# Performance work log

Measured on AMD Instinct MI355X. Metric: run time of the kernel, lower is better.

The kernel has to match this reference:

```python
import jax, jax.numpy as jnp
import numpy as np

NUM_HEADS = 8
NUM_GROUPS = 8
NUM_ITERATIONS = 3
DT = 0.1
EPS = 1e-5


def group_norm(x, scale, bias):
    # x: [B, C, H, W], GroupNorm(8, C)
    B, C, H, W = x.shape
    xg = x.reshape(B, NUM_GROUPS, C // NUM_GROUPS, H, W)
    mean = xg.mean(axis=(2, 3, 4), keepdims=True)
    var = xg.var(axis=(2, 3, 4), keepdims=True)
    xg = (xg - mean) * jax.lax.rsqrt(var + EPS)
    x = xg.reshape(B, C, H, W)
    return x * scale[None, :, None, None] + bias[None, :, None, None]


def setup_inputs() -> dict:
    key = jax.random.key(0)
    ks = jax.random.split(key, 4)
    B, C, H, W = 8, 512, 32, 32
    x = jax.random.normal(ks[0], (B, C, H, W), dtype=jnp.float32)
    qkv_w = jax.random.normal(ks[1], (3 * C, C), dtype=jnp.float32) * (1.0 / np.sqrt(C))
    proj_w = jax.random.normal(ks[2], (C, C), dtype=jnp.float32) * (1.0 / np.sqrt(C))
    inl_w = jax.random.normal(ks[3], (C, C), dtype=jnp.float32) * (1.0 / np.sqrt(C))
    return {
        "x": x,
        "gn_scale": jnp.ones((C,), jnp.float32),
        "gn_bias": jnp.zeros((C,), jnp.float32),
        "qkv_w": qkv_w,
        "qkv_b": jnp.zeros((3 * C,), jnp.float32),
        "proj_w": proj_w,
        "proj_b": jnp.zeros((C,), jnp.float32),
        "inl_w": inl_w,
        "inl_b": jnp.zeros((C,), jnp.float32),
    }


def reference(x, gn_scale, gn_bias, qkv_w, qkv_b, proj_w, proj_b, inl_w, inl_b):
    B, C, H, W = x.shape
    nh = NUM_HEADS
    hd = C // nh
    S = H * W

    h = group_norm(x, gn_scale, gn_bias)

    # 1x1 conv == channel matmul
    qkv = jnp.einsum('oc,bchw->bohw', qkv_w, h) + qkv_b[None, :, None, None]
    q, k, v = jnp.split(qkv, 3, axis=1)  # each [B, C, H, W]

    def to_heads(t):  # [B, C, H, W] -> [B, nh, S, hd]
        return t.reshape(B, nh, hd, S).transpose(0, 1, 3, 2)

    q, k, v = to_heads(q), to_heads(k), to_heads(v)

    scale = hd ** (-0.5)
    attn = jax.nn.softmax(jnp.einsum('bnsd,bntd->bnst', q, k) * scale, axis=-1)
    h = jnp.einsum('bnst,bntd->bnsd', attn, v)  # [B, nh, S, hd]

    # back to [B, S, C] for INL refinement
    h_flat = h.transpose(0, 1, 3, 2).reshape(B, C, S).transpose(0, 2, 1)

    # SimpleINLDynamics: iterative Euler refinement x <- x + dt * tanh(W x + b)
    def step(hf, _):
        hf = hf + DT * jnp.tanh(jnp.einsum('bsc,oc->bso', hf, inl_w) + inl_b)
        return hf, None
    h_flat, _ = jax.lax.scan(step, h_flat, None, length=NUM_ITERATIONS)

    h = h_flat.transpose(0, 2, 1).reshape(B, C, H, W)
    h = jnp.einsum('oc,bchw->bohw', proj_w, h) + proj_b[None, :, None, None]
    return x + h
```

## Files before the change

kernel.cpp:

```cpp
#include <hip/hip_runtime.h>
#include <math.h>

#define B_ 8
#define C_ 512
#define S_ 1024
#define HD 64
#define NHEADS 8
#define NGROUPS 8
#define DT_STEP 0.1f
#define EPS_GN 1e-5f
#define LOG2E 1.4426950408889634f

typedef __attribute__((ext_vector_type(8))) short bf16x8;
typedef __attribute__((ext_vector_type(4))) float f32x4;
typedef __attribute__((ext_vector_type(8))) unsigned short ushort8;
typedef __attribute__((ext_vector_type(4))) unsigned short ushort4_t;

static __device__ __forceinline__ unsigned short f2bf(float f) {
  unsigned int u = __builtin_bit_cast(unsigned int, f);
  u += 0x7fff + ((u >> 16) & 1);
  return (unsigned short)(u >> 16);
}

static __device__ __forceinline__ unsigned short f2bf_fast(float f) {
  unsigned int u = __builtin_bit_cast(unsigned int, f);
  return (unsigned short)((u + 0x8000u) >> 16);
}

static __device__ __forceinline__ float bf2f(unsigned short u) {
  unsigned int t = ((unsigned int)u) << 16;
  return __builtin_bit_cast(float, t);
}

static __device__ __forceinline__ float exp2_raw(float x) {
  return __builtin_amdgcn_exp2f(x);
}

static __device__ __forceinline__ float fast_tanh(float x) {
  float xc = fminf(fmaxf(x, -15.f), 15.f);
  float e = exp2_raw(xc * (2.0f * LOG2E));
  return (e - 1.f) / (e + 1.f);
}

__global__ __launch_bounds__(256) void prep_kernel(
    const float* __restrict__ a, const float* __restrict__ b, const float* __restrict__ c,
    unsigned short* __restrict__ A, unsigned short* __restrict__ B, unsigned short* __restrict__ C,
    const float* __restrict__ x, float* __restrict__ gpart) {
  int bid = blockIdx.x;
  int tid = threadIdx.x;
  if (bid < 384) {
    int off = bid * 2048;
    int i = off + tid * 8;
    f32x4 v0 = *(const f32x4*)(a + i);
    f32x4 v1 = *(const f32x4*)(a + i + 4);
    ushort8 o;
    o[0] = f2bf(v0[0]); o[1] = f2bf(v0[1]); o[2] = f2bf(v0[2]); o[3] = f2bf(v0[3]);
    o[4] = f2bf(v1[0]); o[5] = f2bf(v1[1]); o[6] = f2bf(v1[2]); o[7] = f2bf(v1[3]);
    *(ushort8*)(A + i) = o;
    return;
  }
  if (bid < 640) {
    const float* src; unsigned short* dst; int off;
    if (bid < 512) { src = b; dst = B; off = (bid - 384) * 2048; }
    else { src = c; dst = C; off = (bid - 512) * 2048; }
    int i = off + tid * 8;
    f32x4 v0 = *(const f32x4*)(src + i);
    f32x4 v1 = *(const f32x4*)(src + i + 4);
    ushort8 o;
    o[0] = f2bf(v0[0]); o[1] = f2bf(v0[1]); o[2] = f2bf(v0[2]); o[3] = f2bf(v0[3]);
    o[4] = f2bf(v1[0]); o[5] = f2bf(v1[1]); o[6] = f2bf(v1[2]); o[7] = f2bf(v1[3]);
    int orow = i >> 9, cbase = i & 511;
    int dsti = (cbase >> 5) * 16384 + orow * 32 + (cbase & 31);
    *(ushort8*)(dst + dsti) = o;
    return;
  }
  int sbid = bid - 640;
  int bg = sbid >> 3, chunk = sbid & 7;
  const float* xp = x + (size_t)bg * 65536 + (size_t)chunk * 8192;
  float sum = 0.f, sq = 0.f;
  #pragma unroll
  for (int i = 0; i < 8; ++i) {
    f32x4 v = *(const f32x4*)(xp + i * 1024 + tid * 4);
    sum += v[0] + v[1] + v[2] + v[3];
    sq += v[0]*v[0] + v[1]*v[1] + v[2]*v[2] + v[3]*v[3];
  }
  #pragma unroll
  for (int off = 32; off >= 1; off >>= 1) {
    sum += __shfl_xor(sum, off, 64);
    sq  += __shfl_xor(sq, off, 64);
  }
  __shared__ float s1[4], s2[4];
  int wave = tid >> 6, lane = tid & 63;
  if (lane == 0) { s1[wave] = sum; s2[wave] = sq; }
  __syncthreads();
  if (tid == 0) {
    float S = s1[0] + s1[1] + s1[2] + s1[3];
    float Q = s2[0] + s2[1] + s2[2] + s2[3];
    gpart[bg * 16 + chunk * 2] = S;
    gpart[bg * 16 + chunk * 2 + 1] = Q;
  }
}

__global__ __launch_bounds__(256) void gn_apply_t(
    const float* __restrict__ x, const float* __restrict__ gpart,
    const float* __restrict__ scale, const float* __restrict__ bias,
    unsigned short* __restrict__ h_t) {
  int bid = blockIdx.x;
  int bg = bid >> 4, st = bid & 15;
  int b = bg >> 3, g = bg & 7;
  float S = 0.f, Q = 0.f;
  #pragma unroll
  for (int i = 0; i < 8; ++i) {
    S += gpart[bg * 16 + i * 2];
    Q += gpart[bg * 16 + i * 2 + 1];
  }
  float mean = S / 65536.f;
  float var = Q / 65536.f - mean * mean;
  float inv = rsqrtf(var + EPS_GN);

  int tid = threadIdx.x;
  int sl = tid >> 2;
  int cq = (tid & 3) * 16;
  float sA[16], sB[16];
  #pragma unroll
  for (int u = 0; u < 16; ++u) {
    float scv = scale[g * 64 + cq + u];
    sA[u] = inv * scv;
    sB[u] = bias[g * 64 + cq + u] - mean * inv * scv;
  }

  const float* xp = x + ((size_t)b * C_ + (size_t)g * 64) * S_;
  __shared__ float tile[64][65];
  #pragma unroll
  for (int it = 0; it < 16; ++it) {
    int lin = it * 256 + tid;
    int c = lin >> 6, s = lin & 63;
    tile[c][s] = xp[(size_t)c * S_ + st * 64 + s];
  }
  __syncthreads();
  unsigned short vals[16];
  #pragma unroll
  for (int u = 0; u < 16; ++u)
    vals[u] = f2bf_fast(tile[cq + u][sl] * sA[u] + sB[u]);
  unsigned short* dst = h_t + ((size_t)b * S_ + st * 64 + sl) * C_ + g * 64 + cq;
  ushort8 lo, hi;
  #pragma unroll
  for (int u = 0; u < 8; ++u) { lo[u] = vals[u]; hi[u] = vals[u + 8]; }
  *(ushort8*)dst = lo;
  *(ushort8*)(dst + 8) = hi;
}

template<int MB, int NB, int WMG, int WNG>
__device__ __forceinline__ void gemm_nt_core(
    const unsigned short* __restrict__ Ab,
    const unsigned short* __restrict__ Bb,
    unsigned short* ldsA, unsigned short* ldsB,
    f32x4* acc) {
  constexpr int TI = (MB / WMG) / 16;
  constexpr int TJ = (NB / WNG) / 16;
  constexpr int NQA = MB * 4 / 256;
  constexpr int NQB = NB * 4 / 256;
  const int K = 512;
  const int tid = threadIdx.x;
  const int w = tid >> 6, lane = tid & 63, quad = lane >> 4, l15 = lane & 15;
  const int wm = (WNG == 1) ? w : ((WMG == 1) ? 0 : (w >> 1));
  const int wn = (WNG == 1) ? 0 : ((WMG == 1) ? w : (w & 1));

  ushort8 apf[NQA], bpf[NQB];
  #pragma unroll
  for (int q = 0; q < NQA; ++q) {
    int c = q * 256 + tid;
    apf[q] = *(const ushort8*)(Ab + (size_t)(c >> 2) * K + (c & 3) * 8);
  }
  #pragma unroll
  for (int q = 0; q < NQB; ++q) {
    int c = q * 256 + tid;
    bpf[q] = *(const ushort8*)(Bb + (size_t)(c >> 2) * K + (c & 3) * 8);
  }

  for (int k0 = 0; k0 < K; k0 += 32) {
    __syncthreads();
    #pragma unroll
    for (int q = 0; q < NQA; ++q) {
      int c = q * 256 + tid;
      *(ushort8*)(ldsA + c * 8) = apf[q];
    }
    #pragma unroll
    for (int q = 0; q < NQB; ++q) {
      int c = q * 256 + tid;
      *(ushort8*)(ldsB + c * 8) = bpf[q];
    }
    __syncthreads();
    if (k0 + 32 < K) {
      #pragma unroll
      for (int q = 0; q < NQA; ++q) {
        int c = q * 256 + tid;
        apf[q] = *(const ushort8*)(Ab + (size_t)(c >> 2) * K + k0 + 32 + (c & 3) * 8);
      }
      #pragma unroll
      for (int q = 0; q < NQB; ++q) {
        int c = q * 256 + tid;
        bpf[q] = *(const ushort8*)(Bb + (size_t)(c >> 2) * K + k0 + 32 + (c & 3) * 8);
      }
    }
    bf16x8 af[TI], bfr[TJ];
    #pragma unroll
    for (int i = 0; i < TI; ++i)
      af[i] = *(const bf16x8*)(ldsA + (wm * (MB / WMG) + i * 16 + l15) * 32 + quad * 8);
    #pragma unroll
    for (int j = 0; j < TJ; ++j)
      bfr[j] = *(const bf16x8*)(ldsB + (wn * (NB / WNG) + j * 16 + l15) * 32 + quad * 8);
    #pragma unroll
    for (int i = 0; i < TI; ++i)
      #pragma unroll
      for (int j = 0; j < TJ; ++j)
        acc[i * TJ + j] = __builtin_amdgcn_mfma_f32_16x16x32_bf16(af[i], bfr[j], acc[i * TJ + j], 0, 0, 0);
  }
}

__global__ __launch_bounds__(256) void gemm_qkv_mfma(
    const unsigned short* __restrict__ Wbf, const unsigned short* __restrict__ h_t,
    const float* __restrict__ bias,
    unsigned short* __restrict__ Qt, unsigned short* __restrict__ Kt,
    unsigned short* __restrict__ Vt) {
  __shared__ __align__(16) unsigned short ldsA[128 * 32];
  __shared__ __align__(16) unsigned short ldsB[128 * 32];
  int b = blockIdx.z;
  int bm = blockIdx.y * 128, bn = blockIdx.x * 128;
  f32x4 acc[16];
  #pragma unroll
  for (int t = 0; t < 16; ++t) acc[t] = (f32x4){0.f, 0.f, 0.f, 0.f};
  gemm_nt_core<128, 128, 2, 2>(Wbf + (size_t)bm * 512,
                               h_t + ((size_t)b * S_ + bn) * 512, ldsA, ldsB, acc);
  int tid = threadIdx.x, w = tid >> 6, lane = tid & 63, quad = lane >> 4, l15 = lane & 15;
  int wm = w >> 1, wn = w & 1;
  int tensor = bm >> 9;
  float qscale = (tensor == 0) ? 0.125f * LOG2E : 1.0f;
  #pragma unroll
  for (int i = 0; i < 4; ++i) {
    #pragma unroll
    for (int j = 0; j < 4; ++j) {
      int m0 = bm + wm * 64 + i * 16 + quad * 4;
      int ng = bn + wn * 64 + j * 16 + l15;
      f32x4 v = acc[i * 4 + j];
      if (tensor < 2) {
        int head = (m0 >> 6) & 7, d0 = m0 & 63;
        ushort4_t pk;
        #pragma unroll
        for (int r = 0; r < 4; ++r) pk[r] = f2bf((v[r] + bias[m0 + r]) * qscale);
        unsigned short* dst = (tensor ? Kt : Qt) +
            (((size_t)(b * 8 + head) * S_ + ng) * 64 + d0);
        *(ushort4_t*)dst = pk;
      } else {
        #pragma unroll
        for (int r = 0; r < 4; ++r)
          Vt[(size_t)b * (C_ * S_) + (size_t)(m0 - 1024 + r) * S_ + ng] = f2bf(v[r] + bias[m0 + r]);
      }
    }
  }
}

__global__ __launch_bounds__(256) void attn_mfma(
    const unsigned short* __restrict__ Qt,
    const unsigned short* __restrict__ Kt,
    const unsigned short* __restrict__ Vt,
    unsigned short* __restrict__ hflat_bf) {
  int tid = threadIdx.x, wave = tid >> 6, lane = tid & 63;
  int quad = lane >> 4, l15 = lane & 15;
  int bid = blockIdx.x;
  int bn = bid & 63, sblk = bid >> 6, b = bn >> 3, n = bn & 7;
  int s0w = sblk * 128 + wave * 32;

  __shared__ unsigned short k_lds[64][72];
  __shared__ unsigned short v_lds[64][72];
  __shared__ unsigned short p_lds[4][2][16][72];

  const unsigned short* Kb = Kt + ((size_t)(b * 8 + n)) * S_ * 64;
  const unsigned short* Vb = Vt + ((size_t)b * C_ + n * 64) * S_;

  bf16x8 qa[2][2];
  #pragma unroll
  for (int g = 0; g < 2; ++g) {
    const unsigned short* Qb = Qt + (((size_t)(b * 8 + n)) * S_ + s0w + g * 16 + l15) * 64;
    qa[g][0] = *(const bf16x8*)(Qb + quad * 8);
    qa[g][1] = *(const bf16x8*)(Qb + 32 + quad * 8);
  }

  bf16x8 ones;
  #pragma unroll
  for (int j = 0; j < 8; ++j) ones[j] = (short)0x3F80;

  f32x4 o_acc[2][4];
  f32x4 l_acc[2];
  #pragma unroll
  for (int g = 0; g < 2; ++g) {
    l_acc[g] = (f32x4){0.f, 0.f, 0.f, 0.f};
    #pragma unroll
    for (int dc = 0; dc < 4; ++dc) o_acc[g][dc] = (f32x4){0.f, 0.f, 0.f, 0.f};
  }

  int row0 = tid >> 3, c80 = (tid & 7) * 8;
  int row1 = (tid + 256) >> 3, c81 = c80;

  ushort8 kreg[2], vreg[2];
  kreg[0] = *(const ushort8*)(Kb + (size_t)row0 * 64 + c80);
  kreg[1] = *(const ushort8*)(Kb + (size_t)row1 * 64 + c81);
  vreg[0] = *(const ushort8*)(Vb + (size_t)row0 * S_ + c80);
  vreg[1] = *(const ushort8*)(Vb + (size_t)row1 * S_ + c81);

  for (int t0 = 0; t0 < S_; t0 += 64) {
    __syncthreads();
    *(ushort8*)&k_lds[row0][c80] = kreg[0];
    *(ushort8*)&k_lds[row1][c81] = kreg[1];
    *(ushort8*)&v_lds[row0][c80] = vreg[0];
    *(ushort8*)&v_lds[row1][c81] = vreg[1];
    __syncthreads();
    if (t0 + 64 < S_) {
      int t1 = t0 + 64;
      kreg[0] = *(const ushort8*)(Kb + (size_t)(t1 + row0) * 64 + c80);
      kreg[1] = *(const ushort8*)(Kb + (size_t)(t1 + row1) * 64 + c81);
      vreg[0] = *(const ushort8*)(Vb + (size_t)row0 * S_ + t1 + c80);
      vreg[1] = *(const ushort8*)(Vb + (size_t)row1 * S_ + t1 + c81);
    }

    f32x4 sc[2][4];
    #pragma unroll
    for (int tc = 0; tc < 4; ++tc) {
      bf16x8 kb0 = *(const bf16x8*)&k_lds[tc * 16 + l15][quad * 8];
      bf16x8 kb1 = *(const bf16x8*)&k_lds[tc * 16 + l15][32 + quad * 8];
      #pragma unroll
      for (int g = 0; g < 2; ++g) {
        f32x4 c = {0.f, 0.f, 0.f, 0.f};
        c = __builtin_amdgcn_mfma_f32_16x16x32_bf16(kb0, qa[g][0], c, 0, 0, 0);
        sc[g][tc] = __builtin_amdgcn_mfma_f32_16x16x32_bf16(kb1, qa[g][1], c, 0, 0, 0);
      }
    }

    #pragma unroll
    for (int g = 0; g < 2; ++g)
      #pragma unroll
      for (int tc = 0; tc < 4; ++tc) {
        ushort4_t p4;
        #pragma unroll
        for (int r = 0; r < 4; ++r) p4[r] = f2bf_fast(exp2_raw(sc[g][tc][r]));
        *(ushort4_t*)&p_lds[wave][g][l15][tc * 16 + quad * 4] = p4;
      }

    bf16x8 pa[2][2];
    #pragma unroll
    for (int g = 0; g < 2; ++g) {
      pa[g][0] = *(const bf16x8*)&p_lds[wave][g][l15][quad * 8];
      pa[g][1] = *(const bf16x8*)&p_lds[wave][g][l15][32 + quad * 8];
      l_acc[g] = __builtin_amdgcn_mfma_f32_16x16x32_bf16(pa[g][0], ones, l_acc[g], 0, 0, 0);
      l_acc[g] = __builtin_amdgcn_mfma_f32_16x16x32_bf16(pa[g][1], ones, l_acc[g], 0, 0, 0);
    }
    #pragma unroll
    for (int dc = 0; dc < 4; ++dc) {
      bf16x8 vb0 = *(const bf16x8*)&v_lds[dc * 16 + l15][quad * 8];
      bf16x8 vb1 = *(const bf16x8*)&v_lds[dc * 16 + l15][32 + quad * 8];
      #pragma unroll
      for (int g = 0; g < 2; ++g) {
        o_acc[g][dc] = __builtin_amdgcn_mfma_f32_16x16x32_bf16(pa[g][0], vb0, o_acc[g][dc], 0, 0, 0);
        o_acc[g][dc] = __builtin_amdgcn_mfma_f32_16x16x32_bf16(pa[g][1], vb1, o_acc[g][dc], 0, 0, 0);
      }
    }
  }

  #pragma unroll
  for (int g = 0; g < 2; ++g) {
    float inv_l[4];
    #pragma unroll
    for (int r = 0; r < 4; ++r) inv_l[r] = 1.f / l_acc[g][r];
    #pragma unroll
    for (int dc = 0; dc < 4; ++dc) {
      #pragma unroll
      for (int r = 0; r < 4; ++r) {
        int s = s0w + g * 16 + quad * 4 + r;
        size_t idx = ((size_t)b * S_ + s) * C_ + n * 64 + dc * 16 + l15;
        hflat_bf[idx] = f2bf_fast(o_acc[g][dc][r] * inv_l[r]);
      }
    }
  }
}

__global__ __launch_bounds__(512) void inl_proj_chain(
    const unsigned short* __restrict__ hbf,
    const unsigned short* __restrict__ Wi2,
    const unsigned short* __restrict__ Wp2,
    const float* __restrict__ ib, const float* __restrict__ pb,
    const float* __restrict__ x, float* __restrict__ Out) {
  __shared__ __align__(16) unsigned short h_lds[32][520];

  int tid = threadIdx.x;
  int wave = tid >> 6, lane = tid & 63, quad = lane >> 4, l15 = lane & 15;
  int wo = wave * 64;
  int bid = blockIdx.x;
  int b = bid >> 5, s0 = (bid & 31) * 32;

  const unsigned short* hsrc = hbf + (size_t)bid * 16384;
  #pragma unroll
  for (int it = 0; it < 4; ++it) {
    int lin = it * 512 + tid;
    ushort8 v = *(const ushort8*)(hsrc + (size_t)lin * 8);
    *(ushort8*)&h_lds[lin >> 6][(lin & 63) * 8] = v;
  }

  float bias_i[4], bias_p[4];
  #pragma unroll
  for (int j = 0; j < 4; ++j) {
    bias_i[j] = ib[wo + j * 16 + l15];
    bias_p[j] = pb[wo + j * 16 + l15];
  }

  f32x4 acc[2][4];
  #pragma unroll
  for (int i = 0; i < 2; ++i)
    #pragma unroll
    for (int j = 0; j < 4; ++j) acc[i][j] = (f32x4){0.f, 0.f, 0.f, 0.f};

  __syncthreads();

  for (int step = 0; step < 4; ++step) {
    const unsigned short* Wb = (step < 3) ? Wi2 : Wp2;
    #pragma unroll 4
    for (int slab = 0; slab < 16; ++slab) {
      const unsigned short* wp = Wb + slab * 16384;
      bf16x8 afr[2], bfr[4];
      #pragma unroll
      for (int i = 0; i < 2; ++i)
        afr[i] = *(const bf16x8*)&h_lds[i * 16 + l15][slab * 32 + quad * 8];
      #pragma unroll
      for (int j = 0; j < 4; ++j)
        bfr[j] = *(const bf16x8*)(wp + (size_t)(wo + j * 16 + l15) * 32 + quad * 8);
      #pragma unroll
      for (int i = 0; i < 2; ++i)
        #pragma unroll
        for (int j = 0; j < 4; ++j)
          acc[i][j] = __builtin_amdgcn_mfma_f32_16x16x32_bf16(afr[i], bfr[j], acc[i][j], 0, 0, 0);
    }
    if (step < 3) {
      __syncthreads();
      #pragma unroll
      for (int i = 0; i < 2; ++i)
        #pragma unroll
        for (int j = 0; j < 4; ++j) {
          int o = wo + j * 16 + l15;
          #pragma unroll
          for (int r = 0; r < 4; ++r) {
            int s = i * 16 + quad * 4 + r;
            float hv = bf2f(h_lds[s][o]);
            h_lds[s][o] = f2bf_fast(hv + DT_STEP * fast_tanh(acc[i][j][r] + bias_i[j]));
            acc[i][j][r] = 0.f;
          }
        }
      __syncthreads();
    }
  }

  #pragma unroll
  for (int i = 0; i < 2; ++i)
    #pragma unroll
    for (int j = 0; j < 4; ++j) {
      int o = wo + j * 16 + l15;
      size_t base = (((size_t)b * 512 + o) << 10) + (size_t)(s0 + i * 16 + quad * 4);
      f32x4 xv = *(const f32x4*)(x + base);
      f32x4 ov;
      #pragma unroll
      for (int r = 0; r < 4; ++r) ov[r] = xv[r] + bias_p[j] + acc[i][j][r];
      *(f32x4*)(Out + base) = ov;
    }
}

extern "C" void kernel_launch(void* const* d_in, const int* in_sizes, int n_in,
                              void* d_out, int out_size, void* d_ws, size_t ws_size,
                              hipStream_t stream) {
  const float* x        = (const float*)d_in[0];
  const float* gn_scale = (const float*)d_in[1];
  const float* gn_bias  = (const float*)d_in[2];
  const float* qkv_w    = (const float*)d_in[3];
  const float* qkv_b    = (const float*)d_in[4];
  const float* proj_w   = (const float*)d_in[5];
  const float* proj_b   = (const float*)d_in[6];
  const float* inl_w    = (const float*)d_in[7];
  const float* inl_b    = (const float*)d_in[8];
  float* out = (float*)d_out;
  float* ws = (float*)d_ws;

  unsigned short* Qt  = (unsigned short*)(ws + 8388608);
  unsigned short* Kt  = (unsigned short*)(ws + 10485760);
  unsigned short* Vt  = (unsigned short*)(ws + 12582912);
  unsigned short* h_t = (unsigned short*)(ws + 14680064);
  unsigned short* Abf = (unsigned short*)(ws + 16777216);
  float* gpart = ws + 18874368;
  unsigned short* qkvw_bf  = (unsigned short*)(ws + 18878464);
  unsigned short* inlw_bf  = qkvw_bf + 786432;
  unsigned short* projw_bf = inlw_bf + 262144;

  prep_kernel<<<1152, 256, 0, stream>>>(qkv_w, inl_w, proj_w, qkvw_bf, inlw_bf, projw_bf, x, gpart);
  gn_apply_t<<<1024, 256, 0, stream>>>(x, gpart, gn_scale, gn_bias, h_t);
  gemm_qkv_mfma<<<dim3(8, 12, 8), 256, 0, stream>>>(qkvw_bf, h_t, qkv_b, Qt, Kt, Vt);
  attn_mfma<<<512, 256, 0, stream>>>(Qt, Kt, Vt, Abf);
  inl_proj_chain<<<256, 512, 0, stream>>>(Abf, inlw_bf, projw_bf, inl_b, proj_b, x, out);
}
```

Before: 193.4 us.

## Software-pipeline weight loads across slabs and steps in INL/proj chain kernel

Restructures the INL+projection chain kernel so weight fragments are register-prefetched two slab-pairs ahead, continuously across all four steps including the switch from INL to projection weights. Initial h and weight global loads are issued together before the LDS stores. The step loop is fully unrolled and launch bounds request 2 blocks per CU. The aim is to hide global-memory latency of weight fetches behind MFMA work, at the cost of higher register pressure and larger code size.

```diff
diff --git a/kernel.cpp b/kernel.cpp
--- a/kernel.cpp
+++ b/kernel.cpp
@@ -383,7 +383,17 @@
   }
 }
 
-__global__ __launch_bounds__(512) void inl_proj_chain(
+static __device__ __forceinline__ void loadw4(bf16x8* d, const unsigned short* p) {
+  d[0] = *(const bf16x8*)(p);
+  d[1] = *(const bf16x8*)(p + 512);
+  d[2] = *(const bf16x8*)(p + 1024);
+  d[3] = *(const bf16x8*)(p + 1536);
+}
+static __device__ __forceinline__ void cp4(bf16x8* d, const bf16x8* s) {
+  d[0] = s[0]; d[1] = s[1]; d[2] = s[2]; d[3] = s[3];
+}
+
+__global__ __launch_bounds__(512, 2) void inl_proj_chain(
     const unsigned short* __restrict__ hbf,
     const unsigned short* __restrict__ Wi2,
     const unsigned short* __restrict__ Wp2,
@@ -398,12 +408,18 @@
   int b = bid >> 5, s0 = (bid & 31) * 32;
 
   const unsigned short* hsrc = hbf + (size_t)bid * 16384;
-  #pragma unroll
-  for (int it = 0; it < 4; ++it) {
-    int lin = it * 512 + tid;
-    ushort8 v = *(const ushort8*)(hsrc + (size_t)lin * 8);
-    *(ushort8*)&h_lds[lin >> 6][(lin & 63) * 8] = v;
-  }
+  ushort8 hv0 = *(const ushort8*)(hsrc + (size_t)(tid) * 8);
+  ushort8 hv1 = *(const ushort8*)(hsrc + (size_t)(512 + tid) * 8);
+  ushort8 hv2 = *(const ushort8*)(hsrc + (size_t)(1024 + tid) * 8);
+  ushort8 hv3 = *(const ushort8*)(hsrc + (size_t)(1536 + tid) * 8);
+
+  const int wrow = (wo + l15) * 32 + quad * 8;
+
+  bf16x8 w0[4], w1[4], n0[4], n1[4];
+  loadw4(w0, Wi2 + 0 * 16384 + wrow);
+  loadw4(w1, Wi2 + 1 * 16384 + wrow);
+  loadw4(n0, Wi2 + 2 * 16384 + wrow);
+  loadw4(n1, Wi2 + 3 * 16384 + wrow);
 
   float bias_i[4], bias_p[4];
   #pragma unroll
@@ -412,6 +428,11 @@
     bias_p[j] = pb[wo + j * 16 + l15];
   }
 
+  *(ushort8*)&h_lds[tid >> 6][(tid & 63) * 8] = hv0;
+  { int lin = 512 + tid;  *(ushort8*)&h_lds[lin >> 6][(lin & 63) * 8] = hv1; }
+  { int lin = 1024 + tid; *(ushort8*)&h_lds[lin >> 6][(lin & 63) * 8] = hv2; }
+  { int lin = 1536 + tid; *(ushort8*)&h_lds[lin >> 6][(lin & 63) * 8] = hv3; }
+
   f32x4 acc[2][4];
   #pragma unroll
   for (int i = 0; i < 2; ++i)
@@ -420,23 +441,33 @@
 
   __syncthreads();
 
+  #pragma unroll
   for (int step = 0; step < 4; ++step) {
-    const unsigned short* Wb = (step < 3) ? Wi2 : Wp2;
-    #pragma unroll 4
-    for (int slab = 0; slab < 16; ++slab) {
-      const unsigned short* wp = Wb + slab * 16384;
-      bf16x8 afr[2], bfr[4];
-      #pragma unroll
-      for (int i = 0; i < 2; ++i)
-        afr[i] = *(const bf16x8*)&h_lds[i * 16 + l15][slab * 32 + quad * 8];
-      #pragma unroll
-      for (int j = 0; j < 4; ++j)
-        bfr[j] = *(const bf16x8*)(wp + (size_t)(wo + j * 16 + l15) * 32 + quad * 8);
-      #pragma unroll
-      for (int i = 0; i < 2; ++i)
-        #pragma unroll
-        for (int j = 0; j < 4; ++j)
-          acc[i][j] = __builtin_amdgcn_mfma_f32_16x16x32_bf16(afr[i], bfr[j], acc[i][j], 0, 0, 0);
+    #pragma unroll
+    for (int sp = 0; sp < 8; ++sp) {
+      const int g = step * 16 + sp * 2;
+      bf16x8 p0[4], p1[4];
+      if (g + 4 < 64) {
+        loadw4(p0, ((g + 4) < 48 ? Wi2 : Wp2) + ((g + 4) & 15) * 16384 + wrow);
+        loadw4(p1, ((g + 5) < 48 ? Wi2 : Wp2) + ((g + 5) & 15) * 16384 + wrow);
+      }
+      const int sl0 = sp * 2, sl1 = sp * 2 + 1;
+      bf16x8 a00 = *(const bf16x8*)&h_lds[l15][sl0 * 32 + quad * 8];
+      bf16x8 a10 = *(const bf16x8*)&h_lds[16 + l15][sl0 * 32 + quad * 8];
+      bf16x8 a01 = *(const bf16x8*)&h_lds[l15][sl1 * 32 + quad * 8];
+      bf16x8 a11 = *(const bf16x8*)&h_lds[16 + l15][sl1 * 32 + quad * 8];
+      #pragma unroll
+      for (int j = 0; j < 4; ++j) {
+        acc[0][j] = __builtin_amdgcn_mfma_f32_16x16x32_bf16(a00, w0[j], acc[0][j], 0, 0, 0);
+        acc[1][j] = __builtin_amdgcn_mfma_f32_16x16x32_bf16(a10, w0[j], acc[1][j], 0, 0, 0);
+      }
+      #pragma unroll
+      for (int j = 0; j < 4; ++j) {
+        acc[0][j] = __builtin_amdgcn_mfma_f32_16x16x32_bf16(a01, w1[j], acc[0][j], 0, 0, 0);
+        acc[1][j] = __builtin_amdgcn_mfma_f32_16x16x32_bf16(a11, w1[j], acc[1][j], 0, 0, 0);
+      }
+      cp4(w0, n0); cp4(w1, n1);
+      if (g + 4 < 64) { cp4(n0, p0); cp4(n1, p1); }
     }
     if (step < 3) {
       __syncthreads();
```

New measurement: 189.4 us. 1.02x faster.

## Use 1024-thread blocks and software-prefetch weight slabs in INL/proj chain

Applied to the files above, without the earlier changes.

The INL+projection chain kernel now launches 1024 threads per block, so each wave owns 32 output channels instead of 64. The slab loop is fully unrolled into macros with a 4-deep register prefetch of weight fragments that crosses step boundaries, including into the projection weights. The goal is to hide global-memory latency on weight loads and raise per-CU wave count for the 256-block grid. In exchange it adds register pressure and twice as many waves contending on the barriers between steps.

```diff
diff --git a/kernel.cpp b/kernel.cpp
--- a/kernel.cpp
+++ b/kernel.cpp
@@ -383,7 +383,7 @@
   }
 }
 
-__global__ __launch_bounds__(512) void inl_proj_chain(
+__global__ __launch_bounds__(1024, 4) void inl_proj_chain(
     const unsigned short* __restrict__ hbf,
     const unsigned short* __restrict__ Wi2,
     const unsigned short* __restrict__ Wp2,
@@ -393,82 +393,98 @@
 
   int tid = threadIdx.x;
   int wave = tid >> 6, lane = tid & 63, quad = lane >> 4, l15 = lane & 15;
-  int wo = wave * 64;
+  int wo = wave * 32;
   int bid = blockIdx.x;
   int b = bid >> 5, s0 = (bid & 31) * 32;
 
   const unsigned short* hsrc = hbf + (size_t)bid * 16384;
-  #pragma unroll
-  for (int it = 0; it < 4; ++it) {
-    int lin = it * 512 + tid;
-    ushort8 v = *(const ushort8*)(hsrc + (size_t)lin * 8);
-    *(ushort8*)&h_lds[lin >> 6][(lin & 63) * 8] = v;
-  }
-
-  float bias_i[4], bias_p[4];
-  #pragma unroll
-  for (int j = 0; j < 4; ++j) {
-    bias_i[j] = ib[wo + j * 16 + l15];
-    bias_p[j] = pb[wo + j * 16 + l15];
-  }
-
-  f32x4 acc[2][4];
-  #pragma unroll
-  for (int i = 0; i < 2; ++i)
-    #pragma unroll
-    for (int j = 0; j < 4; ++j) acc[i][j] = (f32x4){0.f, 0.f, 0.f, 0.f};
+  ushort8 hv0 = *(const ushort8*)(hsrc + (size_t)tid * 8);
+  ushort8 hv1 = *(const ushort8*)(hsrc + (size_t)(1024 + tid) * 8);
+
+  const int wrow = (wo + l15) * 32 + quad * 8;
+
+#define PREF_(na, nb, s) { \
+    const unsigned short* wp_ = (((s) < 48) ? Wi2 : Wp2) + ((s) & 15) * 16384 + wrow; \
+    na = *(const bf16x8*)(wp_); \
+    nb = *(const bf16x8*)(wp_ + 512); }
+
+  bf16x8 q0a, q0b, q1a, q1b, q2a, q2b, q3a, q3b;
+  PREF_(q0a, q0b, 0); PREF_(q1a, q1b, 1); PREF_(q2a, q2b, 2); PREF_(q3a, q3b, 3);
+
+  float bi0 = ib[wo + l15], bi1 = ib[wo + 16 + l15];
+  float bp0 = pb[wo + l15], bp1 = pb[wo + 16 + l15];
+
+  *(ushort8*)&h_lds[tid >> 6][(tid & 63) * 8] = hv0;
+  { int lin = 1024 + tid; *(ushort8*)&h_lds[lin >> 6][(lin & 63) * 8] = hv1; }
+
+  f32x4 acc00 = {0.f,0.f,0.f,0.f}, acc01 = {0.f,0.f,0.f,0.f};
+  f32x4 acc10 = {0.f,0.f,0.f,0.f}, acc11 = {0.f,0.f,0.f,0.f};
 
   __syncthreads();
 
-  for (int step = 0; step < 4; ++step) {
-    const unsigned short* Wb = (step < 3) ? Wi2 : Wp2;
-    #pragma unroll 4
-    for (int slab = 0; slab < 16; ++slab) {
-      const unsigned short* wp = Wb + slab * 16384;
-      bf16x8 afr[2], bfr[4];
-      #pragma unroll
-      for (int i = 0; i < 2; ++i)
-        afr[i] = *(const bf16x8*)&h_lds[i * 16 + l15][slab * 32 + quad * 8];
-      #pragma unroll
-      for (int j = 0; j < 4; ++j)
-        bfr[j] = *(const bf16x8*)(wp + (size_t)(wo + j * 16 + l15) * 32 + quad * 8);
-      #pragma unroll
-      for (int i = 0; i < 2; ++i)
-        #pragma unroll
-        for (int j = 0; j < 4; ++j)
-          acc[i][j] = __builtin_amdgcn_mfma_f32_16x16x32_bf16(afr[i], bfr[j], acc[i][j], 0, 0, 0);
-    }
-    if (step < 3) {
-      __syncthreads();
-      #pragma unroll
-      for (int i = 0; i < 2; ++i)
-        #pragma unroll
-        for (int j = 0; j < 4; ++j) {
-          int o = wo + j * 16 + l15;
-          #pragma unroll
-          for (int r = 0; r < 4; ++r) {
-            int s = i * 16 + quad * 4 + r;
-            float hv = bf2f(h_lds[s][o]);
-            h_lds[s][o] = f2bf_fast(hv + DT_STEP * fast_tanh(acc[i][j][r] + bias_i[j]));
-            acc[i][j][r] = 0.f;
-          }
-        }
-      __syncthreads();
-    }
-  }
-
-  #pragma unroll
-  for (int i = 0; i < 2; ++i)
-    #pragma unroll
-    for (int j = 0; j < 4; ++j) {
-      int o = wo + j * 16 + l15;
-      size_t base = (((size_t)b * 512 + o) << 10) + (size_t)(s0 + i * 16 + quad * 4);
-      f32x4 xv = *(const f32x4*)(x + base);
-      f32x4 ov;
-      #pragma unroll
-      for (int r = 0; r < 4; ++r) ov[r] = xv[r] + bias_p[j] + acc[i][j][r];
-      *(f32x4*)(Out + base) = ov;
-    }
+#define DOSLAB_(na, nb, s) { \
+    bf16x8 a0_ = *(const bf16x8*)&h_lds[l15][((s) & 15) * 32 + quad * 8]; \
+    bf16x8 a1_ = *(const bf16x8*)&h_lds[16 + l15][((s) & 15) * 32 + quad * 8]; \
+    acc00 = __builtin_amdgcn_mfma_f32_16x16x32_bf16(a0_, na, acc00, 0, 0, 0); \
+    acc10 = __builtin_amdgcn_mfma_f32_16x16x32_bf16(a1_, na, acc10, 0, 0, 0); \
+    acc01 = __builtin_amdgcn_mfma_f32_16x16x32_bf16(a0_, nb, acc01, 0, 0, 0); \
+    acc11 = __builtin_amdgcn_mfma_f32_16x16x32_bf16(a1_, nb, acc11, 0, 0, 0); }
+
+#define STEP4_(s) \
+    DOSLAB_(q0a, q0b, (s));     if ((s) + 4 < 64) PREF_(q0a, q0b, (s) + 4); \
+    DOSLAB_(q1a, q1b, (s) + 1); if ((s) + 5 < 64) PREF_(q1a, q1b, (s) + 5); \
+    DOSLAB_(q2a, q2b, (s) + 2); if ((s) + 6 < 64) PREF_(q2a, q2b, (s) + 6); \
+    DOSLAB_(q3a, q3b, (s) + 3); if ((s) + 7 < 64) PREF_(q3a, q3b, (s) + 7);
+
+#define UPDATE_ { \
+    __syncthreads(); \
+    _Pragma("unroll") \
+    for (int r = 0; r < 4; ++r) { \
+      int sa = quad * 4 + r, sb = 16 + quad * 4 + r; \
+      int o0 = wo + l15, o1 = wo + 16 + l15; \
+      h_lds[sa][o0] = f2bf_fast(bf2f(h_lds[sa][o0]) + DT_STEP * fast_tanh(acc00[r] + bi0)); \
+      h_lds[sa][o1] = f2bf_fast(bf2f(h_lds[sa][o1]) + DT_STEP * fast_tanh(acc01[r] + bi1)); \
+      h_lds[sb][o0] = f2bf_fast(bf2f(h_lds[sb][o0]) + DT_STEP * fast_tanh(acc10[r] + bi0)); \
+      h_lds[sb][o1] = f2bf_fast(bf2f(h_lds[sb][o1]) + DT_STEP * fast_tanh(acc11[r] + bi1)); \
+    } \
+    acc00 = (f32x4){0.f,0.f,0.f,0.f}; acc01 = (f32x4){0.f,0.f,0.f,0.f}; \
+    acc10 = (f32x4){0.f,0.f,0.f,0.f}; acc11 = (f32x4){0.f,0.f,0.f,0.f}; \
+    __syncthreads(); }
+
+  STEP4_(0); STEP4_(4); STEP4_(8); STEP4_(12);
+  UPDATE_;
+  STEP4_(16); STEP4_(20); STEP4_(24); STEP4_(28);
+  UPDATE_;
+  STEP4_(32); STEP4_(36); STEP4_(40); STEP4_(44);
+  UPDATE_;
+  STEP4_(48); STEP4_(52); STEP4_(56); STEP4_(60);
+
+  {
+    int o0 = wo + l15, o1 = wo + 16 + l15;
+    size_t base0 = (((size_t)b * 512 + o0) << 10) + (size_t)(s0 + quad * 4);
+    size_t base1 = (((size_t)b * 512 + o1) << 10) + (size_t)(s0 + quad * 4);
+    f32x4 xv, ov;
+    xv = *(const f32x4*)(x + base0);
+    #pragma unroll
+    for (int r = 0; r < 4; ++r) ov[r] = xv[r] + bp0 + acc00[r];
+    *(f32x4*)(Out + base0) = ov;
+    xv = *(const f32x4*)(x + base0 + 16);
+    #pragma unroll
+    for (int r = 0; r < 4; ++r) ov[r] = xv[r] + bp0 + acc10[r];
+    *(f32x4*)(Out + base0 + 16) = ov;
+    xv = *(const f32x4*)(x + base1);
+    #pragma unroll
+    for (int r = 0; r < 4; ++r) ov[r] = xv[r] + bp1 + acc01[r];
+    *(f32x4*)(Out + base1) = ov;
+    xv = *(const f32x4*)(x + base1 + 16);
+    #pragma unroll
+    for (int r = 0; r < 4; ++r) ov[r] = xv[r] + bp1 + acc11[r];
+    *(f32x4*)(Out + base1 + 16) = ov;
+  }
+#undef PREF_
+#undef DOSLAB_
+#undef STEP4_
+#undef UPDATE_
 }
 
 extern "C" void kernel_launch(void* const* d_in, const int* in_sizes, int n_in,
@@ -500,5 +516,5 @@
   gn_apply_t<<<1024, 256, 0, stream>>>(x, gpart, gn_scale, gn_bias, h_t);
   gemm_qkv_mfma<<<dim3(8, 12, 8), 256, 0, stream>>>(qkvw_bf, h_t, qkv_b, Qt, Kt, Vt);
   attn_mfma<<<512, 256, 0, stream>>>(Qt, Kt, Vt, Abf);
-  inl_proj_chain<<<256, 512, 0, stream>>>(Abf, inlw_bf, projw_bf, inl_b, proj_b, x, out);
-}
+  inl_proj_chain<<<256, 1024, 0, stream>>>(Abf, inlw_bf, projw_bf, inl_b, proj_b, x, out);
+}
```

Measured after the change: 184.3 us. -4.7%, faster.

## Double-buffer INL weight slabs in LDS via async global-to-LDS loads, 64-row tiles

Applied to the files above, without the earlier changes.

The INL/proj chain kernel now stages each 32-column weight slab into a double-buffered LDS region using global_load_lds, prefetching the next slab while MFMAs run on the current one. The prep kernel XOR-swizzles the weight layout to avoid LDS bank conflicts. Each block now handles 64 sequence rows instead of 32, halving the grid to 128 blocks so each weight slab is reused across more rows. The risks are lower occupancy across the 256 CUs with only 128 blocks, and the manual waitcnt sequencing.

```diff
diff --git a/kernel.cpp b/kernel.cpp
--- a/kernel.cpp
+++ b/kernel.cpp
@@ -40,6 +40,12 @@
   float xc = fminf(fmaxf(x, -15.f), 15.f);
   float e = exp2_raw(xc * (2.0f * LOG2E));
   return (e - 1.f) / (e + 1.f);
+}
+
+static __device__ __forceinline__ void gload_lds16(const unsigned short* g, unsigned short* l) {
+  __builtin_amdgcn_global_load_lds(
+      (const __attribute__((address_space(1))) unsigned int*)g,
+      (__attribute__((address_space(3))) unsigned int*)l, 16, 0, 0);
 }
 
 __global__ __launch_bounds__(256) void prep_kernel(
@@ -70,7 +76,8 @@
     o[0] = f2bf(v0[0]); o[1] = f2bf(v0[1]); o[2] = f2bf(v0[2]); o[3] = f2bf(v0[3]);
     o[4] = f2bf(v1[0]); o[5] = f2bf(v1[1]); o[6] = f2bf(v1[2]); o[7] = f2bf(v1[3]);
     int orow = i >> 9, cbase = i & 511;
-    int dsti = (cbase >> 5) * 16384 + orow * 32 + (cbase & 31);
+    int chunk = ((cbase & 31) >> 3) ^ ((orow >> 1) & 3);
+    int dsti = (cbase >> 5) * 16384 + orow * 32 + chunk * 8;
     *(ushort8*)(dst + dsti) = o;
     return;
   }
@@ -383,92 +390,126 @@
   }
 }
 
-__global__ __launch_bounds__(512) void inl_proj_chain(
+__global__ __launch_bounds__(512, 2) void inl_proj_chain(
     const unsigned short* __restrict__ hbf,
     const unsigned short* __restrict__ Wi2,
     const unsigned short* __restrict__ Wp2,
     const float* __restrict__ ib, const float* __restrict__ pb,
     const float* __restrict__ x, float* __restrict__ Out) {
-  __shared__ __align__(16) unsigned short h_lds[32][520];
+  __shared__ __align__(16) unsigned short h_lds[64][520];
+  __shared__ __align__(16) unsigned short w_lds[2][16384];
 
   int tid = threadIdx.x;
   int wave = tid >> 6, lane = tid & 63, quad = lane >> 4, l15 = lane & 15;
   int wo = wave * 64;
   int bid = blockIdx.x;
-  int b = bid >> 5, s0 = (bid & 31) * 32;
-
-  const unsigned short* hsrc = hbf + (size_t)bid * 16384;
-  #pragma unroll
-  for (int it = 0; it < 4; ++it) {
-    int lin = it * 512 + tid;
-    ushort8 v = *(const ushort8*)(hsrc + (size_t)lin * 8);
-    *(ushort8*)&h_lds[lin >> 6][(lin & 63) * 8] = v;
-  }
-
-  float bias_i[4], bias_p[4];
+  int b = bid >> 4, s0 = (bid & 15) * 64;
+
+  const unsigned short* hsrc = hbf + (size_t)bid * 32768;
+  ushort8 hv[8];
+  #pragma unroll
+  for (int q = 0; q < 8; ++q)
+    hv[q] = *(const ushort8*)(hsrc + (size_t)(q * 512 + tid) * 8);
+
+  float bi[4], bp[4];
   #pragma unroll
   for (int j = 0; j < 4; ++j) {
-    bias_i[j] = ib[wo + j * 16 + l15];
-    bias_p[j] = pb[wo + j * 16 + l15];
-  }
-
-  f32x4 acc[2][4];
-  #pragma unroll
-  for (int i = 0; i < 2; ++i)
+    bi[j] = ib[wo + j * 16 + l15];
+    bp[j] = pb[wo + j * 16 + l15];
+  }
+
+  #pragma unroll
+  for (int q = 0; q < 8; ++q) {
+    int lin = q * 512 + tid;
+    *(ushort8*)&h_lds[lin >> 6][(lin & 63) * 8] = hv[q];
+  }
+
+  f32x4 acc[4][4];
+  #pragma unroll
+  for (int i = 0; i < 4; ++i)
     #pragma unroll
     for (int j = 0; j < 4; ++j) acc[i][j] = (f32x4){0.f, 0.f, 0.f, 0.f};
 
+  int o_[4];
+  #pragma unroll
+  for (int j = 0; j < 4; ++j) o_[j] = wo + j * 16 + l15;
+  const int wofs = wave * 2048;
+  const int lofs = lane * 8;
+  const int wcol = (quad ^ ((l15 >> 1) & 3)) * 8;
+
   __syncthreads();
 
+#define ISSUE_(base, slab, buf) { \
+    const unsigned short* ws_ = (base) + (slab) * 16384 + wofs; \
+    gload_lds16(ws_ + lofs, &w_lds[buf][wofs]); \
+    gload_lds16(ws_ + 512 + lofs, &w_lds[buf][wofs + 512]); \
+    gload_lds16(ws_ + 1024 + lofs, &w_lds[buf][wofs + 1024]); \
+    gload_lds16(ws_ + 1536 + lofs, &w_lds[buf][wofs + 1536]); }
+
+  ISSUE_(Wi2, 0, 0);
+
+  #pragma unroll
   for (int step = 0; step < 4; ++step) {
-    const unsigned short* Wb = (step < 3) ? Wi2 : Wp2;
-    #pragma unroll 4
-    for (int slab = 0; slab < 16; ++slab) {
-      const unsigned short* wp = Wb + slab * 16384;
-      bf16x8 afr[2], bfr[4];
-      #pragma unroll
-      for (int i = 0; i < 2; ++i)
-        afr[i] = *(const bf16x8*)&h_lds[i * 16 + l15][slab * 32 + quad * 8];
+    #pragma unroll
+    for (int s = 0; s < 16; ++s) {
+      const int g = step * 16 + s;
+      const int cur = g & 1;
+      asm volatile("s_waitcnt lgkmcnt(0)" ::: "memory");
+      if (g + 1 < 64) {
+        const unsigned short* nb_ = ((g + 1) < 48) ? Wi2 : Wp2;
+        ISSUE_(nb_, (g + 1) & 15, cur ^ 1);
+        asm volatile("s_waitcnt vmcnt(4)" ::: "memory");
+      } else {
+        asm volatile("s_waitcnt vmcnt(0)" ::: "memory");
+      }
+
+      const int kb = s * 32 + quad * 8;
+      bf16x8 a[4], w[4];
+      #pragma unroll
+      for (int i = 0; i < 4; ++i)
+        a[i] = *(const bf16x8*)&h_lds[i * 16 + l15][kb];
       #pragma unroll
       for (int j = 0; j < 4; ++j)
-        bfr[j] = *(const bf16x8*)(wp + (size_t)(wo + j * 16 + l15) * 32 + quad * 8);
-      #pragma unroll
-      for (int i = 0; i < 2; ++i)
+        w[j] = *(const bf16x8*)&w_lds[cur][o_[j] * 32 + wcol];
+      #pragma unroll
+      for (int i = 0; i < 4; ++i)
         #pragma unroll
         for (int j = 0; j < 4; ++j)
-          acc[i][j] = __builtin_amdgcn_mfma_f32_16x16x32_bf16(afr[i], bfr[j], acc[i][j], 0, 0, 0);
-    }
+          acc[i][j] = __builtin_amdgcn_mfma_f32_16x16x32_bf16(a[i], w[j], acc[i][j], 0, 0, 0);
+    }
+
     if (step < 3) {
       __syncthreads();
       #pragma unroll
-      for (int i = 0; i < 2; ++i)
+      for (int i = 0; i < 4; ++i)
         #pragma unroll
-        for (int j = 0; j < 4; ++j) {
-          int o = wo + j * 16 + l15;
+        for (int j = 0; j < 4; ++j)
           #pragma unroll
           for (int r = 0; r < 4; ++r) {
-            int s = i * 16 + quad * 4 + r;
-            float hv = bf2f(h_lds[s][o]);
-            h_lds[s][o] = f2bf_fast(hv + DT_STEP * fast_tanh(acc[i][j][r] + bias_i[j]));
-            acc[i][j][r] = 0.f;
+            int srow = i * 16 + quad * 4 + r;
+            h_lds[srow][o_[j]] =
+                f2bf_fast(bf2f(h_lds[srow][o_[j]]) + DT_STEP * fast_tanh(acc[i][j][r] + bi[j]));
           }
-        }
+      #pragma unroll
+      for (int i = 0; i < 4; ++i)
+        #pragma unroll
+        for (int j = 0; j < 4; ++j) acc[i][j] = (f32x4){0.f, 0.f, 0.f, 0.f};
       __syncthreads();
     }
   }
 
   #pragma unroll
-  for (int i = 0; i < 2; ++i)
+  for (int i = 0; i < 4; ++i)
     #pragma unroll
     for (int j = 0; j < 4; ++j) {
-      int o = wo + j * 16 + l15;
-      size_t base = (((size_t)b * 512 + o) << 10) + (size_t)(s0 + i * 16 + quad * 4);
-      f32x4 xv = *(const f32x4*)(x + base);
+      size_t base_ = (((size_t)b * 512 + o_[j]) << 10) + (size_t)(s0 + i * 16 + quad * 4);
+      f32x4 xv = *(const f32x4*)(x + base_);
       f32x4 ov;
       #pragma unroll
-      for (int r = 0; r < 4; ++r) ov[r] = xv[r] + bias_p[j] + acc[i][j][r];
-      *(f32x4*)(Out + base) = ov;
-    }
+      for (int r = 0; r < 4; ++r) ov[r] = xv[r] + bp[j] + acc[i][j][r];
+      *(f32x4*)(Out + base_) = ov;
+    }
+#undef ISSUE_
 }
 
 extern "C" void kernel_launch(void* const* d_in, const int* in_sizes, int n_in,
@@ -500,5 +541,5 @@
   gn_apply_t<<<1024, 256, 0, stream>>>(x, gpart, gn_scale, gn_bias, h_t);
   gemm_qkv_mfma<<<dim3(8, 12, 8), 256, 0, stream>>>(qkvw_bf, h_t, qkv_b, Qt, Kt, Vt);
   attn_mfma<<<512, 256, 0, stream>>>(Qt, Kt, Vt, Abf);
-  inl_proj_chain<<<256, 512, 0, stream>>>(Abf, inlw_bf, projw_bf, inl_b, proj_b, x, out);
-}
+  inl_proj_chain<<<128, 512, 0, stream>>>(Abf, inlw_bf, projw_bf, inl_b, proj_b, x, out);
+}
```

Result: no change. 194.6 us (+0.6%).
